# Optimization experiments

Measured on AMD Instinct MI355X. Metric: run time of the kernel, lower is better.

## Reference

```python
import jax, jax.numpy as jnp
import numpy as np

RADIUS = 5  # kernels_radius -> diameter 11, 121 window taps
KERNELS_DESC = [
    {"weight": 0.9, "xy": 6.0, "rgb": 0.1},  # RGBXY kernel
    {"weight": 0.1, "xy": 6.0},               # XY kernel
]


def _unfold(img, r):
    # img: [N, C, H, W] -> [N, C, d, d, H, W] with zero padding (== F.unfold semantics)
    N, C, H, W = img.shape
    d = 2 * r + 1
    p = jnp.pad(img, ((0, 0), (0, 0), (r, r), (r, r)))
    patches = jnp.stack(
        [p[:, :, dy:dy + H, dx:dx + W] for dy in range(d) for dx in range(d)], axis=2
    )
    return patches.reshape(N, C, d, d, H, W)


def _get_mesh(N, H, W, dtype):
    xs = jnp.broadcast_to(jnp.arange(W, dtype=dtype).reshape(1, 1, 1, W), (N, 1, H, W))
    ys = jnp.broadcast_to(jnp.arange(H, dtype=dtype).reshape(1, 1, H, 1), (N, 1, H, W))
    return jnp.concatenate((xs, ys), axis=1)  # [N, 2, H, W]


def _kernel_from_features(features, r):
    # features: [N, C, H, W] -> Gaussian affinity [N, 1, d, d, H, W], center zeroed
    N, C, H, W = features.shape
    k = _unfold(features, r)                         # [N, C, d, d, H, W]
    center = k[:, :, r, r, :, :][:, :, None, None]   # [N, C, 1, 1, H, W]
    k = jnp.exp(jnp.sum(-0.5 * (k - center) ** 2, axis=1, keepdims=True))
    k = k.at[:, :, r, r, :, :].set(0.0)
    return k


def _forward(y_hat_softmax, rgb):
    N, C, H, W = y_hat_softmax.shape
    # adaptive_avg_pool2d 256->128 is an exact 2x2 mean pool
    _, Cr, Hi, Wi = rgb.shape
    rgb_ds = rgb.reshape(N, Cr, H, Hi // H, W, Wi // W).mean(axis=(3, 5))
    mesh = _get_mesh(N, H, W, y_hat_softmax.dtype)

    kernels = None
    for desc in KERNELS_DESC:
        feats = []
        for modality, sigma in desc.items():
            if modality == "weight":
                continue
            f = mesh if modality == "xy" else rgb_ds
            feats.append(f / jnp.asarray(sigma, y_hat_softmax.dtype))
        features = jnp.concatenate(feats, axis=1)
        k = desc["weight"] * _kernel_from_features(features, RADIUS)
        kernels = k if kernels is None else kernels + k

    denom = N * H * W
    d = 2 * RADIUS + 1
    y_unf = _unfold(y_hat_softmax, RADIUS)                       # [N, C, d, d, H, W]
    prod = (kernels * y_unf).reshape(N, C, d * d, H, W).sum(axis=2)  # [N, C, H, W]
    loss = kernels.sum() - (prod * y_hat_softmax).sum()
    return loss / denom


def setup_inputs() -> dict:
    key = jax.random.key(0)
    k1, k2 = jax.random.split(key)
    logits = jax.random.normal(k1, (2, 21, 128, 128), dtype=jnp.float32)
    y_hat_softmax = jax.nn.softmax(logits, axis=1)
    rgb = jax.random.uniform(k2, (2, 3, 256, 256), dtype=jnp.float32)
    return {"y_hat_softmax": y_hat_softmax, "rgb": rgb}


def reference(y_hat_softmax, rgb):
    return _forward(y_hat_softmax, rgb)
```

## Files before the change

kernel.cpp:

```cpp
#include <hip/hip_runtime.h>

#define RAD   5
#define DIA   11
#define IMH   128
#define IMW   128
#define NCH   21
#define TILE  8
#define SW    18
#define SP    324

__global__ __launch_bounds__(256)
void crf_loss_kernel(const float* __restrict__ y, const float* __restrict__ rgb,
                     float* __restrict__ out) {
    __shared__ float4 ys4[SP * 7];
    __shared__ float4 ftA[SP];
    __shared__ float  ftB[SP];
    __shared__ float  wred[4];

    const int tid = threadIdx.x;
    const int b   = blockIdx.x;
    const int tx0 = (b & 15) * TILE;
    const int ty0 = ((b >> 4) & 15) * TILE;
    const int n   = b >> 8;

    const int x0 = tx0 - RAD, y0 = ty0 - RAD;

    for (int i = tid; i < SP; i += 256) {
        int sy = i / SW, sx = i - sy * SW;
        int gx = x0 + sx, gy = y0 + sy;
        float fx = 0.f, fy = 0.f, cr = 0.f, cg = 0.f, cb = 0.f;
        if (gx >= 0 && gx < IMW && gy >= 0 && gy < IMH) {
            fx = (float)gx * (1.0f / 6.0f);
            fy = (float)gy * (1.0f / 6.0f);
            const int cs = 256 * 256;
            const float* rp = rgb + ((n * 3) * cs + (2 * gy) * 256 + 2 * gx);
            cr = (rp[0]      + rp[1]        + rp[256]      + rp[257])      * 2.5f;
            cg = (rp[cs]     + rp[cs + 1]   + rp[cs + 256] + rp[cs + 257]) * 2.5f;
            cb = (rp[2*cs]   + rp[2*cs + 1] + rp[2*cs+256] + rp[2*cs+257]) * 2.5f;
        }
        ftA[i] = make_float4(fx, fy, cr, cg);
        ftB[i] = cb;
    }

    for (int i = tid; i < SP * 6; i += 256) {
        int cg4 = i / SP, px = i - cg4 * SP;
        int sy = px / SW, sx = px - sy * SW;
        int gx = x0 + sx, gy = y0 + sy;
        float4 v = make_float4(0.f, 0.f, 0.f, 0.f);
        if (gx >= 0 && gx < IMW && gy >= 0 && gy < IMH) {
            const float* yp = y + ((n * NCH) << 14) + (gy << 7) + gx;
            int c0 = cg4 * 4;
            v.x = yp[(c0 + 0) << 14];
            if (c0 + 1 < NCH) v.y = yp[(c0 + 1) << 14];
            if (c0 + 2 < NCH) v.z = yp[(c0 + 2) << 14];
            if (c0 + 3 < NCH) v.w = yp[(c0 + 3) << 14];
        }
        ys4[px * 7 + cg4] = v;
    }
    __syncthreads();

    const int px  = tid & 63;
    const int grp = tid >> 6;
    const int lx  = px & 7, ly = px >> 3;
    const int ci  = (ly + RAD) * SW + (lx + RAD);

    const float4* ycp = ys4 + ci * 7;
    const float4 c0 = ycp[0], c1 = ycp[1], c2 = ycp[2],
                 c3 = ycp[3], c4 = ycp[4], c5 = ycp[5];
    const float4 fA = ftA[ci];
    const float  fB = ftB[ci];

    float acc = 0.f;
    int dx = grp, dy = 0;
    for (int t = grp; t < 121; t += 4) {
        const int nb = (ly + dy) * SW + (lx + dx);

        const float4 nA = ftA[nb];
        const float  nB = ftB[nb];
        const float dfx = fA.x - nA.x, dfy = fA.y - nA.y;
        const float dr  = fA.z - nA.z, dg  = fA.w - nA.w, db = fB - nB;
        const float sxy  = dfx * dfx + dfy * dfy;
        const float srgb = dr * dr + dg * dg + db * db;
        float K = __expf(-0.5f * sxy) * (0.9f * __expf(-0.5f * srgb) + 0.1f);
        K = (t == 60) ? 0.0f : K;

        const float4* yn = ys4 + nb * 7;
        const float4 a0 = yn[0], a1 = yn[1], a2 = yn[2],
                     a3 = yn[3], a4 = yn[4], a5 = yn[5];
        float dot;
        dot  = a0.x * c0.x + a0.y * c0.y + a0.z * c0.z + a0.w * c0.w;
        dot += a1.x * c1.x + a1.y * c1.y + a1.z * c1.z + a1.w * c1.w;
        dot += a2.x * c2.x + a2.y * c2.y + a2.z * c2.z + a2.w * c2.w;
        dot += a3.x * c3.x + a3.y * c3.y + a3.z * c3.z + a3.w * c3.w;
        dot += a4.x * c4.x + a4.y * c4.y + a4.z * c4.z + a4.w * c4.w;
        dot += a5.x * c5.x + a5.y * c5.y + a5.z * c5.z + a5.w * c5.w;

        acc += K * (1.0f - dot);

        dx += 4; if (dx >= DIA) { dx -= DIA; dy += 1; }
    }

    for (int off = 32; off > 0; off >>= 1) acc += __shfl_down(acc, off);
    if ((tid & 63) == 0) wred[tid >> 6] = acc;
    __syncthreads();
    if (tid == 0) {
        float s = (wred[0] + wred[1] + wred[2] + wred[3]) * (1.0f / 32768.0f);
        atomicAdd(out, s);
    }
}

extern "C" void kernel_launch(void* const* d_in, const int* in_sizes, int n_in,
                              void* d_out, int out_size, void* d_ws, size_t ws_size,
                              hipStream_t stream) {
    const float* y   = (const float*)d_in[0];
    const float* rgb = (const float*)d_in[1];
    float* out = (float*)d_out;

    hipMemsetAsync(out, 0, sizeof(float), stream);
    crf_loss_kernel<<<dim3(2 * 16 * 16), dim3(256), 0, stream>>>(y, rgb, out);
}
```

Before: 77.71 us.

## Precompute spatial Gaussian table, pack RGB into padded channel slot, split reduction

Precomputes the spatial (xy) Gaussian weights and neighbor offsets per tap in shared memory, so interior tiles avoid one exp and the position-feature loads. RGB features are packed into the unused lanes of the last channel float4, which removes a separate feature array read. Boundary tiles keep the full computation. The memset plus atomic add is replaced by per-block partials in workspace and a second finalize kernel. This adds a kernel launch and some code duplication.

```diff
diff --git a/kernel.cpp b/kernel.cpp
--- a/kernel.cpp
+++ b/kernel.cpp
@@ -8,13 +8,15 @@
 #define TILE  8
 #define SW    18
 #define SP    324
+#define NBLK  512
 
 __global__ __launch_bounds__(256)
-void crf_loss_kernel(const float* __restrict__ y, const float* __restrict__ rgb,
-                     float* __restrict__ out) {
+void crf_partial(const float* __restrict__ y, const float* __restrict__ rgb,
+                 float* __restrict__ ws) {
     __shared__ float4 ys4[SP * 7];
-    __shared__ float4 ftA[SP];
-    __shared__ float  ftB[SP];
+    __shared__ float2 fxy[SP];
+    __shared__ float  wtab[128];
+    __shared__ int    otab[128];
     __shared__ float  wred[4];
 
     const int tid = threadIdx.x;
@@ -22,24 +24,26 @@
     const int tx0 = (b & 15) * TILE;
     const int ty0 = ((b >> 4) & 15) * TILE;
     const int n   = b >> 8;
+    const int x0  = tx0 - RAD, y0 = ty0 - RAD;
+    const bool interior = (x0 >= 0) & (y0 >= 0) & (x0 + SW <= IMW) & (y0 + SW <= IMH);
 
-    const int x0 = tx0 - RAD, y0 = ty0 - RAD;
+    if (tid < 121) {
+        int dy = tid / DIA, dx = tid - dy * DIA;
+        float ddx = (dx - RAD) * (1.0f / 6.0f);
+        float ddy = (dy - RAD) * (1.0f / 6.0f);
+        wtab[tid] = (tid == 60) ? 0.0f : __expf(-0.5f * (ddx * ddx + ddy * ddy));
+        otab[tid] = (dy - RAD) * SW + (dx - RAD);
+    }
 
     for (int i = tid; i < SP; i += 256) {
         int sy = i / SW, sx = i - sy * SW;
         int gx = x0 + sx, gy = y0 + sy;
-        float fx = 0.f, fy = 0.f, cr = 0.f, cg = 0.f, cb = 0.f;
+        float fx = 0.f, fy = 0.f;
         if (gx >= 0 && gx < IMW && gy >= 0 && gy < IMH) {
             fx = (float)gx * (1.0f / 6.0f);
             fy = (float)gy * (1.0f / 6.0f);
-            const int cs = 256 * 256;
-            const float* rp = rgb + ((n * 3) * cs + (2 * gy) * 256 + 2 * gx);
-            cr = (rp[0]      + rp[1]        + rp[256]      + rp[257])      * 2.5f;
-            cg = (rp[cs]     + rp[cs + 1]   + rp[cs + 256] + rp[cs + 257]) * 2.5f;
-            cb = (rp[2*cs]   + rp[2*cs + 1] + rp[2*cs+256] + rp[2*cs+257]) * 2.5f;
         }
-        ftA[i] = make_float4(fx, fy, cr, cg);
-        ftB[i] = cb;
+        fxy[i] = make_float2(fx, fy);
     }
 
     for (int i = tid; i < SP * 6; i += 256) {
@@ -49,11 +53,20 @@
         float4 v = make_float4(0.f, 0.f, 0.f, 0.f);
         if (gx >= 0 && gx < IMW && gy >= 0 && gy < IMH) {
             const float* yp = y + ((n * NCH) << 14) + (gy << 7) + gx;
-            int c0 = cg4 * 4;
-            v.x = yp[(c0 + 0) << 14];
-            if (c0 + 1 < NCH) v.y = yp[(c0 + 1) << 14];
-            if (c0 + 2 < NCH) v.z = yp[(c0 + 2) << 14];
-            if (c0 + 3 < NCH) v.w = yp[(c0 + 3) << 14];
+            if (cg4 < 5) {
+                int c0 = cg4 * 4;
+                v.x = yp[(c0 + 0) << 14];
+                v.y = yp[(c0 + 1) << 14];
+                v.z = yp[(c0 + 2) << 14];
+                v.w = yp[(c0 + 3) << 14];
+            } else {
+                v.x = yp[20 << 14];
+                const int cs = 256 * 256;
+                const float* rp = rgb + ((n * 3) * cs + (gy << 9) + (gx << 1));
+                v.y = (rp[0]      + rp[1]        + rp[256]      + rp[257])      * 2.5f;
+                v.z = (rp[cs]     + rp[cs + 1]   + rp[cs + 256] + rp[cs + 257]) * 2.5f;
+                v.w = (rp[2*cs]   + rp[2*cs + 1] + rp[2*cs+256] + rp[2*cs+257]) * 2.5f;
+            }
         }
         ys4[px * 7 + cg4] = v;
     }
@@ -67,46 +80,64 @@
     const float4* ycp = ys4 + ci * 7;
     const float4 c0 = ycp[0], c1 = ycp[1], c2 = ycp[2],
                  c3 = ycp[3], c4 = ycp[4], c5 = ycp[5];
-    const float4 fA = ftA[ci];
-    const float  fB = ftB[ci];
+    const float2 cf = fxy[ci];
 
     float acc = 0.f;
-    int dx = grp, dy = 0;
-    for (int t = grp; t < 121; t += 4) {
-        const int nb = (ly + dy) * SW + (lx + dx);
-
-        const float4 nA = ftA[nb];
-        const float  nB = ftB[nb];
-        const float dfx = fA.x - nA.x, dfy = fA.y - nA.y;
-        const float dr  = fA.z - nA.z, dg  = fA.w - nA.w, db = fB - nB;
-        const float sxy  = dfx * dfx + dfy * dfy;
-        const float srgb = dr * dr + dg * dg + db * db;
-        float K = __expf(-0.5f * sxy) * (0.9f * __expf(-0.5f * srgb) + 0.1f);
-        K = (t == 60) ? 0.0f : K;
-
-        const float4* yn = ys4 + nb * 7;
-        const float4 a0 = yn[0], a1 = yn[1], a2 = yn[2],
-                     a3 = yn[3], a4 = yn[4], a5 = yn[5];
-        float dot;
-        dot  = a0.x * c0.x + a0.y * c0.y + a0.z * c0.z + a0.w * c0.w;
-        dot += a1.x * c1.x + a1.y * c1.y + a1.z * c1.z + a1.w * c1.w;
-        dot += a2.x * c2.x + a2.y * c2.y + a2.z * c2.z + a2.w * c2.w;
-        dot += a3.x * c3.x + a3.y * c3.y + a3.z * c3.z + a3.w * c3.w;
-        dot += a4.x * c4.x + a4.y * c4.y + a4.z * c4.z + a4.w * c4.w;
-        dot += a5.x * c5.x + a5.y * c5.y + a5.z * c5.z + a5.w * c5.w;
-
-        acc += K * (1.0f - dot);
-
-        dx += 4; if (dx >= DIA) { dx -= DIA; dy += 1; }
+    if (interior) {
+        for (int t = grp; t < 121; t += 4) {
+            const int nb = ci + otab[t];
+            const float4* yn = ys4 + nb * 7;
+            const float4 a0 = yn[0], a1 = yn[1], a2 = yn[2],
+                         a3 = yn[3], a4 = yn[4], a5 = yn[5];
+            const float dr = c5.y - a5.y, dg = c5.z - a5.z, db = c5.w - a5.w;
+            const float K  = wtab[t] * (0.9f * __expf(-0.5f * (dr*dr + dg*dg + db*db)) + 0.1f);
+            float dot;
+            dot  = a0.x * c0.x + a0.y * c0.y + a0.z * c0.z + a0.w * c0.w;
+            dot += a1.x * c1.x + a1.y * c1.y + a1.z * c1.z + a1.w * c1.w;
+            dot += a2.x * c2.x + a2.y * c2.y + a2.z * c2.z + a2.w * c2.w;
+            dot += a3.x * c3.x + a3.y * c3.y + a3.z * c3.z + a3.w * c3.w;
+            dot += a4.x * c4.x + a4.y * c4.y + a4.z * c4.z + a4.w * c4.w;
+            dot += a5.x * c5.x;
+            acc += K * (1.0f - dot);
+        }
+    } else {
+        for (int t = grp; t < 121; t += 4) {
+            const int nb = ci + otab[t];
+            const float4* yn = ys4 + nb * 7;
+            const float2 nf = fxy[nb];
+            const float4 a0 = yn[0], a1 = yn[1], a2 = yn[2],
+                         a3 = yn[3], a4 = yn[4], a5 = yn[5];
+            const float dfx = cf.x - nf.x, dfy = cf.y - nf.y;
+            const float dr  = c5.y - a5.y, dg = c5.z - a5.z, db = c5.w - a5.w;
+            float K = __expf(-0.5f * (dfx*dfx + dfy*dfy)) *
+                      (0.9f * __expf(-0.5f * (dr*dr + dg*dg + db*db)) + 0.1f);
+            K = (t == 60) ? 0.0f : K;
+            float dot;
+            dot  = a0.x * c0.x + a0.y * c0.y + a0.z * c0.z + a0.w * c0.w;
+            dot += a1.x * c1.x + a1.y * c1.y + a1.z * c1.z + a1.w * c1.w;
+            dot += a2.x * c2.x + a2.y * c2.y + a2.z * c2.z + a2.w * c2.w;
+            dot += a3.x * c3.x + a3.y * c3.y + a3.z * c3.z + a3.w * c3.w;
+            dot += a4.x * c4.x + a4.y * c4.y + a4.z * c4.z + a4.w * c4.w;
+            dot += a5.x * c5.x;
+            acc += K * (1.0f - dot);
+        }
     }
 
     for (int off = 32; off > 0; off >>= 1) acc += __shfl_down(acc, off);
     if ((tid & 63) == 0) wred[tid >> 6] = acc;
     __syncthreads();
-    if (tid == 0) {
-        float s = (wred[0] + wred[1] + wred[2] + wred[3]) * (1.0f / 32768.0f);
-        atomicAdd(out, s);
-    }
+    if (tid == 0) ws[b] = wred[0] + wred[1] + wred[2] + wred[3];
+}
+
+__global__ __launch_bounds__(256)
+void crf_finalize(const float* __restrict__ ws, float* __restrict__ out) {
+    __shared__ float wred[4];
+    const int tid = threadIdx.x;
+    float v = ws[tid] + ws[tid + 256];
+    for (int off = 32; off > 0; off >>= 1) v += __shfl_down(v, off);
+    if ((tid & 63) == 0) wred[tid >> 6] = v;
+    __syncthreads();
+    if (tid == 0) out[0] = (wred[0] + wred[1] + wred[2] + wred[3]) * (1.0f / 32768.0f);
 }
 
 extern "C" void kernel_launch(void* const* d_in, const int* in_sizes, int n_in,
@@ -115,7 +146,8 @@
     const float* y   = (const float*)d_in[0];
     const float* rgb = (const float*)d_in[1];
     float* out = (float*)d_out;
+    float* ws  = (float*)d_ws;
 
-    hipMemsetAsync(out, 0, sizeof(float), stream);
-    crf_loss_kernel<<<dim3(2 * 16 * 16), dim3(256), 0, stream>>>(y, rgb, out);
+    crf_partial<<<dim3(NBLK), dim3(256), 0, stream>>>(y, rgb, ws);
+    crf_finalize<<<dim3(1), dim3(256), 0, stream>>>(ws, out);
 }
```

After: 72.03 us. 7.3% less time.
